# Kernel optimization log

Measured on AMD Instinct MI355X. Metric: run time of the kernel, lower is better.

Reference implementation:

```python
import jax, jax.numpy as jnp
import numpy as np

N, K, C0, H = 256, 16, 16, 32  # vertices, regular degree, input feats, hidden


def setup_inputs() -> dict:
    key = jax.random.key(0)
    ks = jax.random.split(key, 4)
    # k-regular circulant graph: neighbors of i are i+/-1..i+/-K//2 (mod N), sorted by vertex id
    offs = np.concatenate([np.arange(1, K // 2 + 1), -np.arange(1, K // 2 + 1)])
    nbrs = np.sort((np.arange(N)[:, None] + offs[None, :]) % N, axis=1).astype(np.int32)
    X = jax.random.normal(ks[0], (N, C0), jnp.float32)
    W1 = jax.random.normal(ks[1], (18 * C0, H), jnp.float32) / np.sqrt(18 * C0)
    b1 = jnp.zeros((H,), jnp.float32)
    W2 = jax.random.normal(ks[2], (18 * H, H), jnp.float32) / np.sqrt(18 * H)
    b2 = jnp.zeros((H,), jnp.float32)
    fc_w = jax.random.normal(ks[3], (H, 1), jnp.float32) / np.sqrt(H)
    fc_b = jnp.zeros((1,), jnp.float32)
    return {"X": X, "nbrs": jnp.asarray(nbrs), "W1": W1, "b1": b1,
            "W2": W2, "b2": b2, "fc_w": fc_w, "fc_b": fc_b}


def contract18(T, A):
    """All 18 contractions of F6[t,a,b,e,f,c] = T[t,a,b,c] * A[e,f],
    exactly matching _collapse6to3 (_c6to2_111 + _c6to2_12 + _c6to2_3),
    without materializing the 6-d tensor.
    T: (n, k, k, k, c) with axes (vertex, t, a, b, channel); A: (k, k).
    Returns (n, k, k, 18*c)."""
    S = A.sum()            # total sum of A
    r = A.sum(1)           # row sums
    tr = jnp.trace(A)
    sum_b = T.sum(3)              # (n,t,a,c)
    sum_t = T.sum(1)              # (n,a,b,c)
    sum_ab = T.sum((2, 3))        # (n,t,c)
    sum_tb = T.sum((1, 3))        # (n,a,c)
    sum_all = T.sum((1, 2, 3))    # (n,c)
    # _c6to2_111 (5 permutations)
    c1 = sum_b * S
    c2 = sum_ab[:, :, None, :] * r[None, None, :, None]
    c3 = sum_t * S
    c4 = sum_tb[:, :, None, :] * r[None, None, :, None]
    c5 = sum_all[:, None, None, :] * A[None, :, :, None]
    # _c6to2_12 (1 nontrivial permutation + 9 identical identity permutations)
    c6 = jnp.einsum('ntabc,b->ntac', T, r)
    c7 = sum_b * tr  # repeated 9 times, as in the source
    # _c6to2_3 (3 planar-diagonal contractions)
    d_ab = jnp.diagonal(T, axis1=2, axis2=3).transpose(0, 1, 3, 2)   # (n,t,a,c): T[t,a,a,c]
    c16 = jnp.einsum('ntac,ea->ntec', d_ab, A)
    d_tb = jnp.diagonal(T, axis1=1, axis2=3)                          # (n,a,c,t): T[t,a,t,c]
    c17 = jnp.einsum('nact,et->naec', d_tb, A)
    d_ttt = jnp.einsum('ntttc->ntc', T).sum(1)                        # (n,c)
    c18 = d_ttt[:, None, None, :] * A[None, :, :, None]
    return jnp.concatenate([c1, c2, c3, c4, c5, c6] + [c7] * 9 + [c16, c17, c18], axis=-1)


def _forward(X, nbrs, W1, b1, W2, b2, fc_w, fc_b):
    n, k = nbrs.shape
    # chi_{i,t}[a,p] = 1 iff a-th neighbor of i == p-th neighbor of j, j = nbrs[i,t]
    NN = nbrs[nbrs]                                                    # (n,k,k)
    CH = (nbrs[:, None, :, None] == NN[:, :, None, :]).astype(X.dtype)  # (n,t,a,p)
    A = jnp.eye(k, dtype=X.dtype)  # chi_{i,i} is the k x k identity for every i

    # get_F0: broadcast vertex features to (n, k, k, c0)
    F = jnp.broadcast_to(X[:, None, None, :], (n, k, k, X.shape[1]))

    def layer(F, W, b):
        Fg = F[nbrs]                                             # (n,t,p,q,c) gather neighbor features
        tmp = jnp.einsum('ntap,ntpqc->ntaqc', CH, Fg)            # chi @ F
        T = jnp.einsum('ntaqc,ntbq->ntabc', tmp, CH)             # (chi @ F) @ chi^T
        col = contract18(T, A)                                   # (n,k,k,18c)
        return jax.nn.relu(col @ W + b)

    F1 = layer(F, W1, b1)
    F2 = layer(F1, W2, b2)
    # get_Troot then full sum: chi_root scatters F2 entries injectively into [n,n,c],
    # so sum over Troot == sum over all entries of F2.
    g = F2.sum((0, 1, 2))                                        # (H,)
    return g @ fc_w + fc_b                                       # (1,)


def reference(X, nbrs, W1, b1, W2, b2, fc_w, fc_b):
    return _forward(X, nbrs, W1, b1, W2, b2, fc_w, fc_b)
```

## Files before the change

### kernel.cpp

```cpp
#include <hip/hip_runtime.h>


constexpr int KN = 16, HH = 32, NV = 256, C2 = 32;

#define MM_SL(WPTR, NB, COEF_EXPR, ACC) do {                                   \
    const float4* W4_ = (const float4*)(WPTR);                                 \
    _Pragma("unroll")                                                          \
    for (int B = 0; B < (NB); ++B) {                                           \
        _Pragma("unroll")                                                      \
        for (int cc = 0; cc < 8; ++cc) {                                       \
            const int ci = B * 8 + cc;                                         \
            const float cf_ = (COEF_EXPR);                                     \
            _Pragma("unroll")                                                  \
            for (int h4 = 0; h4 < 8; ++h4) {                                   \
                const float4 w_ = W4_[ci * 8 + h4];                            \
                (ACC)[4*h4+0] = fmaf(cf_, w_.x, (ACC)[4*h4+0]);                \
                (ACC)[4*h4+1] = fmaf(cf_, w_.y, (ACC)[4*h4+1]);                \
                (ACC)[4*h4+2] = fmaf(cf_, w_.z, (ACC)[4*h4+2]);                \
                (ACC)[4*h4+3] = fmaf(cf_, w_.w, (ACC)[4*h4+3]);                \
            }                                                                  \
        }                                                                      \
    }                                                                          \
} while (0)

__global__ __launch_bounds__(512)
void ccn_l1(const float* __restrict__ X, const int* __restrict__ nbrs,
            const float* __restrict__ W1, const float* __restrict__ bias,
            float* __restrict__ F1c, float* __restrict__ outz,
            const float* __restrict__ W2f, float* __restrict__ Wsb2)
{
    __shared__ float sE1[6 * 512];
    __shared__ float sPP2[8 * 256 * 4];
    __shared__ float sX[16][20];
    __shared__ float sV[16][164];
    __shared__ int   s_nbi[16];
    __shared__ int   s_nbj[16][17];
    __shared__ int   s_P[16][16];
    __shared__ int   s_vm[16];
    __shared__ float s_m[16];

    const int tid  = threadIdx.x;
    const int i    = ((blockIdx.x & 7) << 5) | (blockIdx.x >> 3);

    if (blockIdx.x == 0 && tid == 0) outz[0] = 0.f;

    if (blockIdx.x < 2) {
        const int u = (blockIdx.x << 9) | tid;
        float acc = 0.f;
        #pragma unroll
        for (int g = 6; g < 15; ++g) acc += W2f[g * 1024 + u];
        Wsb2[u] = 16.f * W2f[u] + W2f[5 * 1024 + u] + 16.f * acc;
    }

    if (tid < 16) s_nbi[tid] = nbrs[i * 16 + tid];
    __syncthreads();

    if (tid < 256) {
        const int t = tid >> 4, y = tid & 15;
        const int j = s_nbi[t];
        s_nbj[t][y] = nbrs[j * 16 + y];
        sX[t][y]    = X[j * 16 + y];
    } else {
        const int u = tid - 256;
        float acc = 0.f;
        #pragma unroll
        for (int g = 6; g < 15; ++g) acc += W1[g * 512 + u];
        sE1[u]        = 16.f * W1[u] + W1[5 * 512 + u] + 16.f * acc;
        sE1[512 + u]  = W1[512 + u];
        sE1[1024 + u] = W1[15 * 512 + u];
        sE1[2048 + u] = W1[3 * 512 + u];
        sE1[2560 + u] = W1[4 * 512 + u];
    }
    __syncthreads();

    if (tid < 256) {
        const int t = tid >> 4, y = tid & 15;
        const int tgt = s_nbi[y];
        int p = -1;
        #pragma unroll
        for (int q = 0; q < 16; ++q) if (s_nbj[t][q] == tgt) p = q;
        s_P[t][y] = p;
        unsigned long long bal = __ballot(p >= 0);
        if (y == 0) {
            int vm = (int)((bal >> ((t & 3) * 16)) & 0xFFFFull);
            s_vm[t] = vm;
            s_m[t]  = (float)__popc(vm);
        }
    } else {
        const int u = tid;
        float acc = 0.f;
        #pragma unroll
        for (int g = 6; g < 15; ++g) acc += W1[g * 512 + u];
        sE1[u]        = 16.f * W1[u] + W1[5 * 512 + u] + 16.f * acc;
        sE1[512 + u]  = W1[512 + u];
        sE1[1024 + u] = W1[15 * 512 + u];
        sE1[2048 + u] = W1[3 * 512 + u];
        sE1[2560 + u] = W1[4 * 512 + u];
    }
    __syncthreads();

    if (tid < 256) {
        const int t = tid >> 4, y = tid & 15, x = t;
        float Y0[16];
        #pragma unroll
        for (int c4 = 0; c4 < 4; ++c4) {
            float4 v = *(const float4*)&sX[t][4 * c4];
            Y0[4*c4+0] = v.x; Y0[4*c4+1] = v.y; Y0[4*c4+2] = v.z; Y0[4*c4+3] = v.w;
        }
        float Z4[16], Z5[16];
        #pragma unroll
        for (int c = 0; c < 16; ++c) { Z4[c] = 0.f; Z5[c] = 0.f; }
        #pragma unroll
        for (int tp = 0; tp < 16; ++tp) {
            const int vm = s_vm[tp];
            const float mt = s_m[tp];
            const float fb = ((vm >> x) & 1) ? mt : 0.f;
            const float f5 = mt * mt;
            #pragma unroll
            for (int c4 = 0; c4 < 4; ++c4) {
                float4 v = *(const float4*)&sX[tp][4 * c4];
                Z4[4*c4+0] = fmaf(fb, v.x, Z4[4*c4+0]);
                Z4[4*c4+1] = fmaf(fb, v.y, Z4[4*c4+1]);
                Z4[4*c4+2] = fmaf(fb, v.z, Z4[4*c4+2]);
                Z4[4*c4+3] = fmaf(fb, v.w, Z4[4*c4+3]);
                Z5[4*c4+0] = fmaf(f5, v.x, Z5[4*c4+0]);
                Z5[4*c4+1] = fmaf(f5, v.y, Z5[4*c4+1]);
                Z5[4*c4+2] = fmaf(f5, v.z, Z5[4*c4+2]);
                Z5[4*c4+3] = fmaf(f5, v.w, Z5[4*c4+3]);
            }
        }
        const float m = s_m[t];
        float v0a=0.f,v0b=0.f,v1a=0.f,v1b=0.f,v2a=0.f,v2b=0.f;
        float v3a=0.f,v3b=0.f,v4a=0.f,v4b=0.f;
        const float2* Wsb = (const float2*)(sE1 + 0 * 512);
        const float2* Wab = (const float2*)(sE1 + 1 * 512);
        const float2* W16 = (const float2*)(sE1 + 2 * 512);
        const float2* Wtb = (const float2*)(sE1 + 4 * 512);
        const float2* Wal = (const float2*)(sE1 + 5 * 512);
        #pragma unroll
        for (int c = 0; c < 16; ++c) {
            const float cf0 = m * Y0[c];
            const float cf1 = m * cf0;
            const float cf2 = Y0[c];
            const float cf3 = Z4[c];
            const float cf4 = Z5[c];
            const int idx = c * 16 + y;
            float2 w0 = Wsb[idx]; v0a = fmaf(cf0, w0.x, v0a); v0b = fmaf(cf0, w0.y, v0b);
            float2 w1 = Wab[idx]; v1a = fmaf(cf1, w1.x, v1a); v1b = fmaf(cf1, w1.y, v1b);
            float2 w2 = W16[idx]; v2a = fmaf(cf2, w2.x, v2a); v2b = fmaf(cf2, w2.y, v2b);
            float2 w3 = Wtb[idx]; v3a = fmaf(cf3, w3.x, v3a); v3b = fmaf(cf3, w3.y, v3b);
            float2 w4 = Wal[idx]; v4a = fmaf(cf4, w4.x, v4a); v4b = fmaf(cf4, w4.y, v4b);
        }
        *(float2*)&sV[t][0 * 32 + 2 * y] = make_float2(v0a, v0b);
        *(float2*)&sV[t][1 * 32 + 2 * y] = make_float2(v1a, v1b);
        *(float2*)&sV[t][2 * 32 + 2 * y] = make_float2(v2a, v2b);
        *(float2*)&sV[t][3 * 32 + 2 * y] = make_float2(v3a, v3b);
        *(float2*)&sV[t][4 * 32 + 2 * y] = make_float2(v4a, v4b);
    } else {
        const int w = tid - 256;
        const int t = w >> 4, y = w & 15, x = t;
        float Z2[16];
        #pragma unroll
        for (int c = 0; c < 16; ++c) Z2[c] = 0.f;
        #pragma unroll
        for (int tp = 0; tp < 16; ++tp) {
            const int vm = s_vm[tp];
            const float f2 = (float)((vm >> x) & (vm >> y) & 1);
            #pragma unroll
            for (int c4 = 0; c4 < 4; ++c4) {
                float4 v = *(const float4*)&sX[tp][4 * c4];
                Z2[4*c4+0] = fmaf(f2, v.x, Z2[4*c4+0]);
                Z2[4*c4+1] = fmaf(f2, v.y, Z2[4*c4+1]);
                Z2[4*c4+2] = fmaf(f2, v.z, Z2[4*c4+2]);
                Z2[4*c4+3] = fmaf(f2, v.w, Z2[4*c4+3]);
            }
        }
        float pp[HH];
        #pragma unroll
        for (int h = 0; h < HH; ++h) pp[h] = 0.f;
        MM_SL(W1 + 2 * 512, 2, 16.f * Z2[ci], pp);
        const int cell = y * 16 + t;
        #pragma unroll
        for (int h4 = 0; h4 < 8; ++h4)
            *(float4*)&sPP2[(h4 * 256 + cell) * 4] =
                make_float4(pp[4*h4], pp[4*h4+1], pp[4*h4+2], pp[4*h4+3]);
    }
    __syncthreads();

    if (tid < 256) {
        const int q = tid >> 4, p = tid & 15;
        const float vy  = (s_P[p][q] >= 0) ? 1.f : 0.f;
        const float dxy = (p == q) ? 1.f : 0.f;
        float4* F4 = (float4*)F1c;
        const size_t basec = ((size_t)i * 16 + q) * 128 + p;
        #pragma unroll
        for (int h4 = 0; h4 < 8; ++h4) {
            const float4 V0 = *(const float4*)&sV[p][0 * 32 + 4 * h4];
            const float4 V1 = *(const float4*)&sV[p][1 * 32 + 4 * h4];
            const float4 V2 = *(const float4*)&sV[p][2 * 32 + 4 * h4];
            const float4 V3 = *(const float4*)&sV[p][3 * 32 + 4 * h4];
            const float4 V4 = *(const float4*)&sV[p][4 * 32 + 4 * h4];
            const float4 PP = *(const float4*)&sPP2[(h4 * 256 + q * 16 + p) * 4];
            float a_ = vy*(V0.x+V2.x) + V1.x + V3.x + dxy*V4.x + PP.x + bias[4*h4+0];
            float b_ = vy*(V0.y+V2.y) + V1.y + V3.y + dxy*V4.y + PP.y + bias[4*h4+1];
            float c_ = vy*(V0.z+V2.z) + V1.z + V3.z + dxy*V4.z + PP.z + bias[4*h4+2];
            float d_ = vy*(V0.w+V2.w) + V1.w + V3.w + dxy*V4.w + PP.w + bias[4*h4+3];
            F4[basec + h4 * 16] = make_float4(a_ > 0.f ? a_ : 0.f, b_ > 0.f ? b_ : 0.f,
                                              c_ > 0.f ? c_ : 0.f, d_ > 0.f ? d_ : 0.f);
        }
    }
}

__global__ __launch_bounds__(512)
void ccn_l2(const float* __restrict__ F1c, const int* __restrict__ nbrs,
            const float* __restrict__ W2, const float* __restrict__ bias,
            const float* __restrict__ fcw, const float* __restrict__ fcb,
            float* __restrict__ out, const float* __restrict__ Wsb2)
{
    __shared__ float sW3[3 * 1024];
    __shared__ float sRpp[256 * 36];
    __shared__ float s_stb[16 * 33];
    __shared__ float s_sall[C2];
    __shared__ int   s_nbi[16];
    __shared__ int   s_PQ[16 * 17];
    __shared__ float s_red[4];

    const int tid  = threadIdx.x;
    const int i    = ((blockIdx.x & 7) << 5) | (blockIdx.x >> 3);
    const int lane = tid & 63;
    const float4* F4 = (const float4*)F1c;

    if (tid < 16) s_nbi[tid] = nbrs[i * 16 + tid];
    __syncthreads();

    if (tid < 256) {
        const int t = tid >> 4, y = tid & 15;
        const int j = s_nbi[t];
        s_PQ[t * 17 + y] = nbrs[j * 16 + y];
    } else {
        const int w = tid - 256;
        #pragma unroll
        for (int s = 0; s < 4; ++s) {
            const int u = w + s * 256;
            sW3[u]        = W2[1 * 1024 + u];
            sW3[1024 + u] = W2[3 * 1024 + u];
            sW3[2048 + u] = W2[4 * 1024 + u];
        }
    }
    __syncthreads();

    if (tid < 256) {
        const int t = tid >> 4, y = tid & 15;
        const int tgt = s_nbi[y];
        int p = -1;
        #pragma unroll
        for (int q = 0; q < 16; ++q) if (s_PQ[t * 17 + q] == tgt) p = q;
        s_PQ[t * 17 + y] = p;
    }
    __syncthreads();

    float pre[HH];
    float sab[C2];
    float pp[HH];

    if (tid < 256) {
        const int t = tid >> 4, y = tid & 15;
        const int j = s_nbi[t];
        const int p = s_PQ[t * 17 + y];
        const float mp = (p >= 0) ? 1.f : 0.f;
        const int pc = p >= 0 ? p : 0;
        const size_t jbase = (size_t)j * 2048;

        float R[C2];
        #pragma unroll
        for (int c = 0; c < C2; ++c) R[c] = 0.f;
        #pragma unroll
        for (int b = 0; b < 16; ++b) {
            const int q = s_PQ[t * 17 + b];
            const float mm = (q >= 0) ? mp : 0.f;
            const int qc = q >= 0 ? q : 0;
            const size_t rb = jbase + (size_t)qc * 128 + pc;
            #pragma unroll
            for (int c4 = 0; c4 < 8; ++c4) {
                float4 v = F4[rb + c4 * 16];
                R[4*c4+0] = fmaf(mm, v.x, R[4*c4+0]);
                R[4*c4+1] = fmaf(mm, v.y, R[4*c4+1]);
                R[4*c4+2] = fmaf(mm, v.z, R[4*c4+2]);
                R[4*c4+3] = fmaf(mm, v.w, R[4*c4+3]);
            }
        }
        #pragma unroll
        for (int c4 = 0; c4 < 8; ++c4)
            *(float4*)&sRpp[(t * 16 + y) * 36 + 4 * c4] =
                make_float4(R[4*c4+0], R[4*c4+1], R[4*c4+2], R[4*c4+3]);

        #pragma unroll
        for (int h = 0; h < HH; ++h) pre[h] = 0.f;
        MM_SL(Wsb2, 4, R[ci], pre);

        #pragma unroll
        for (int c = 0; c < C2; ++c) {
            float s = R[c];
            s += __shfl_xor(s, 1);
            s += __shfl_xor(s, 2);
            s += __shfl_xor(s, 4);
            s += __shfl_xor(s, 8);
            sab[c] = s;
        }

        float D[C2];
        {
            const size_t db = jbase + (size_t)pc * 128 + pc;
            #pragma unroll
            for (int c4 = 0; c4 < 8; ++c4) {
                float4 v = F4[db + c4 * 16];
                D[4*c4+0] = mp * v.x; D[4*c4+1] = mp * v.y;
                D[4*c4+2] = mp * v.z; D[4*c4+3] = mp * v.w;
            }
        }
        MM_SL(W2 + 15 * 1024, 4, D[ci], pre);
    } else {
        const int w = tid - 256;
        const int g = w >> 4, l = w & 15;
        float ST[C2];
        #pragma unroll
        for (int c = 0; c < C2; ++c) ST[c] = 0.f;
        #pragma unroll
        for (int tp = 0; tp < 16; ++tp) {
            const int jt = s_nbi[tp];
            const int py = s_PQ[tp * 17 + g];
            const int px = s_PQ[tp * 17 + l];
            const float mm = (px >= 0 && py >= 0) ? 1.f : 0.f;
            const int pyc = py >= 0 ? py : 0;
            const int pxc = px >= 0 ? px : 0;
            const size_t rb = (size_t)jt * 2048 + (size_t)pyc * 128 + pxc;
            #pragma unroll
            for (int c4 = 0; c4 < 8; ++c4) {
                float4 v = F4[rb + c4 * 16];
                ST[4*c4+0] = fmaf(mm, v.x, ST[4*c4+0]);
                ST[4*c4+1] = fmaf(mm, v.y, ST[4*c4+1]);
                ST[4*c4+2] = fmaf(mm, v.z, ST[4*c4+2]);
                ST[4*c4+3] = fmaf(mm, v.w, ST[4*c4+3]);
            }
        }
        #pragma unroll
        for (int h = 0; h < HH; ++h) pp[h] = 0.f;
        MM_SL(W2 + 2 * 1024, 4, 16.f * ST[ci], pp);
    }
    __syncthreads();

    if (tid < 256) {
        #pragma unroll
        for (int k = 0; k < 2; ++k) {
            const int x2 = (tid >> 5) + 8 * k;
            const int c = tid & 31;
            float s = 0.f;
            #pragma unroll
            for (int tt = 0; tt < 16; ++tt) s += sRpp[(tt * 16 + x2) * 36 + c];
            s_stb[x2 * 33 + c] = s;
        }
    }
    __syncthreads();

    if (tid < 256) {
        if (tid < 32) {
            float s = 0.f;
            #pragma unroll
            for (int x2 = 0; x2 < 16; ++x2) s += s_stb[x2 * 33 + tid];
            s_sall[tid] = s;
        }
    } else {
        const int w = tid - 256;
        const int g = w >> 4, l = w & 15;
        float* dst = &sRpp[(l * 16 + g) * 36];
        #pragma unroll
        for (int h4 = 0; h4 < 8; ++h4)
            *(float4*)&dst[4 * h4] = make_float4(pp[4*h4], pp[4*h4+1], pp[4*h4+2], pp[4*h4+3]);
    }
    __syncthreads();

    if (tid < 256) {
        const int t = tid >> 4, y = tid & 15, x = t;
        const float dxy = (x == y) ? 1.f : 0.f;
        float S0 = 0.f, S1 = 0.f, L0 = 0.f, L1 = 0.f;
        {
            const float2* Wab = (const float2*)(sW3 + 0 * 1024);
            const float2* Wtb = (const float2*)(sW3 + 1 * 1024);
            const float2* Wal = (const float2*)(sW3 + 2 * 1024);
            #pragma unroll
            for (int c = 0; c < C2; ++c) {
                const float cfa = sab[c];
                const float cft = s_stb[t * 33 + c];
                const float cfl = s_sall[c];
                const int idx = c * 16 + y;
                float2 wa = Wab[idx]; S0 = fmaf(cfa, wa.x, S0); S1 = fmaf(cfa, wa.y, S1);
                float2 wt = Wtb[idx]; S0 = fmaf(cft, wt.x, S0); S1 = fmaf(cft, wt.y, S1);
                float2 wl = Wal[idx]; L0 = fmaf(cfl, wl.x, L0); L1 = fmaf(cfl, wl.y, L1);
            }
        }
        const int gbase = (t & 3) * 16;
        #pragma unroll
        for (int h = 0; h < HH; ++h) {
            const int src = gbase + (h >> 1);
            const float sv = (h & 1) ? S1 : S0;
            const float lv = (h & 1) ? L1 : L0;
            pre[h] += __shfl(sv, src, 64) + dxy * __shfl(lv, src, 64);
        }
        {
            const float* ppr = &sRpp[(t * 16 + y) * 36];
            #pragma unroll
            for (int h4 = 0; h4 < 8; ++h4) {
                const float4 v = *(const float4*)&ppr[4 * h4];
                pre[4*h4+0] += v.x; pre[4*h4+1] += v.y;
                pre[4*h4+2] += v.z; pre[4*h4+3] += v.w;
            }
        }
        float local = 0.f;
        #pragma unroll
        for (int h = 0; h < HH; ++h) {
            float v = pre[h] + bias[h];
            v = v > 0.f ? v : 0.f;
            local += v * fcw[h];
        }
        #pragma unroll
        for (int off = 32; off > 0; off >>= 1) local += __shfl_down(local, off, 64);
        if (lane == 0) s_red[tid >> 6] = local;
    }
    __syncthreads();
    if (tid == 0) {
        const float v = s_red[0] + s_red[1] + s_red[2] + s_red[3]
                      + fcb[0] * (1.f / 256.f);
        atomicAdd(out, v);
    }
}

extern "C" void kernel_launch(void* const* d_in, const int* in_sizes, int n_in,
                              void* d_out, int out_size, void* d_ws, size_t ws_size,
                              hipStream_t stream) {
    const float* X    = (const float*)d_in[0];
    const int*   nbrs = (const int*)  d_in[1];
    const float* W1   = (const float*)d_in[2];
    const float* b1   = (const float*)d_in[3];
    const float* W2   = (const float*)d_in[4];
    const float* b2   = (const float*)d_in[5];
    const float* fc_w = (const float*)d_in[6];
    const float* fc_b = (const float*)d_in[7];
    float* outp = (float*)d_out;

    float* F1c  = (float*)d_ws;
    float* Wsb2 = F1c + 2097152;

    ccn_l1<<<NV, 512, 0, stream>>>(X, nbrs, W1, b1, F1c, outp, W2, Wsb2);
    ccn_l2<<<NV, 512, 0, stream>>>(F1c, nbrs, W2, b2, fc_w, fc_b, outp, Wsb2);
}
```

Measured before the change: 113.6 us.

## Use packed FP32 FMA and stage weight matrices in shared memory

The scalar fmaf accumulation loops in both kernels become v_pk_fma/add/mul_f32 inline assembly on float2 vectors, which halves the VALU instruction count for the dense accumulations. The weight slices consumed by the MM_SL matmuls (W1 block 2, Wsb2, W2 blocks 15 and 2) are now copied into LDS up front and read from there instead of from global memory. This trades more shared memory per block, which may lower occupancy, for less global traffic and fewer arithmetic instructions. Inline asm can also limit how the compiler schedules and allocates registers.

```diff
diff --git a/kernel.cpp b/kernel.cpp
--- a/kernel.cpp
+++ b/kernel.cpp
@@ -3,22 +3,38 @@
 
 constexpr int KN = 16, HH = 32, NV = 256, C2 = 32;
 
-#define MM_SL(WPTR, NB, COEF_EXPR, ACC) do {                                   \
-    const float4* W4_ = (const float4*)(WPTR);                                 \
+typedef float f32x2 __attribute__((ext_vector_type(2)));
+typedef float f32x4 __attribute__((ext_vector_type(4)));
+
+__device__ __forceinline__ f32x2 pkfma(f32x2 a, f32x2 b, f32x2 c) {
+    f32x2 d;
+    asm("v_pk_fma_f32 %0, %1, %2, %3" : "=v"(d) : "v"(a), "v"(b), "v"(c));
+    return d;
+}
+__device__ __forceinline__ f32x2 pkadd(f32x2 a, f32x2 b) {
+    f32x2 d;
+    asm("v_pk_add_f32 %0, %1, %2" : "=v"(d) : "v"(a), "v"(b));
+    return d;
+}
+__device__ __forceinline__ f32x2 pkmul(f32x2 a, f32x2 b) {
+    f32x2 d;
+    asm("v_pk_mul_f32 %0, %1, %2" : "=v"(d) : "v"(a), "v"(b));
+    return d;
+}
+__device__ __forceinline__ f32x2 vlo(f32x4 v) { return __builtin_shufflevector(v, v, 0, 1); }
+__device__ __forceinline__ f32x2 vhi(f32x4 v) { return __builtin_shufflevector(v, v, 2, 3); }
+
+#define MM_DS(WLDS, NC, COEF_EXPR, ACC2) do {                                  \
+    const f32x4* W4_ = (const f32x4*)(WLDS);                                   \
     _Pragma("unroll")                                                          \
-    for (int B = 0; B < (NB); ++B) {                                           \
+    for (int ci = 0; ci < (NC); ++ci) {                                        \
+        const float cfs_ = (COEF_EXPR);                                        \
+        const f32x2 cf2_ = {cfs_, cfs_};                                       \
         _Pragma("unroll")                                                      \
-        for (int cc = 0; cc < 8; ++cc) {                                       \
-            const int ci = B * 8 + cc;                                         \
-            const float cf_ = (COEF_EXPR);                                     \
-            _Pragma("unroll")                                                  \
-            for (int h4 = 0; h4 < 8; ++h4) {                                   \
-                const float4 w_ = W4_[ci * 8 + h4];                            \
-                (ACC)[4*h4+0] = fmaf(cf_, w_.x, (ACC)[4*h4+0]);                \
-                (ACC)[4*h4+1] = fmaf(cf_, w_.y, (ACC)[4*h4+1]);                \
-                (ACC)[4*h4+2] = fmaf(cf_, w_.z, (ACC)[4*h4+2]);                \
-                (ACC)[4*h4+3] = fmaf(cf_, w_.w, (ACC)[4*h4+3]);                \
-            }                                                                  \
+        for (int h4 = 0; h4 < 8; ++h4) {                                       \
+            const f32x4 w_ = W4_[ci * 8 + h4];                                 \
+            (ACC2)[2*h4+0] = pkfma(cf2_, vlo(w_), (ACC2)[2*h4+0]);             \
+            (ACC2)[2*h4+1] = pkfma(cf2_, vhi(w_), (ACC2)[2*h4+1]);             \
         }                                                                      \
     }                                                                          \
 } while (0)
@@ -68,6 +84,7 @@
         sE1[u]        = 16.f * W1[u] + W1[5 * 512 + u] + 16.f * acc;
         sE1[512 + u]  = W1[512 + u];
         sE1[1024 + u] = W1[15 * 512 + u];
+        sE1[1536 + u] = W1[2 * 512 + u];
         sE1[2048 + u] = W1[3 * 512 + u];
         sE1[2560 + u] = W1[4 * 512 + u];
     }
@@ -94,6 +111,7 @@
         sE1[u]        = 16.f * W1[u] + W1[5 * 512 + u] + 16.f * acc;
         sE1[512 + u]  = W1[512 + u];
         sE1[1024 + u] = W1[15 * 512 + u];
+        sE1[1536 + u] = W1[2 * 512 + u];
         sE1[2048 + u] = W1[3 * 512 + u];
         sE1[2560 + u] = W1[4 * 512 + u];
     }
@@ -107,26 +125,24 @@
             float4 v = *(const float4*)&sX[t][4 * c4];
             Y0[4*c4+0] = v.x; Y0[4*c4+1] = v.y; Y0[4*c4+2] = v.z; Y0[4*c4+3] = v.w;
         }
-        float Z4[16], Z5[16];
-        #pragma unroll
-        for (int c = 0; c < 16; ++c) { Z4[c] = 0.f; Z5[c] = 0.f; }
+        f32x2 Z42[8], Z52[8];
+        #pragma unroll
+        for (int c = 0; c < 8; ++c) { Z42[c] = (f32x2){0.f,0.f}; Z52[c] = (f32x2){0.f,0.f}; }
         #pragma unroll
         for (int tp = 0; tp < 16; ++tp) {
             const int vm = s_vm[tp];
             const float mt = s_m[tp];
             const float fb = ((vm >> x) & 1) ? mt : 0.f;
             const float f5 = mt * mt;
+            const f32x2 fb2 = {fb, fb};
+            const f32x2 f52 = {f5, f5};
             #pragma unroll
             for (int c4 = 0; c4 < 4; ++c4) {
-                float4 v = *(const float4*)&sX[tp][4 * c4];
-                Z4[4*c4+0] = fmaf(fb, v.x, Z4[4*c4+0]);
-                Z4[4*c4+1] = fmaf(fb, v.y, Z4[4*c4+1]);
-                Z4[4*c4+2] = fmaf(fb, v.z, Z4[4*c4+2]);
-                Z4[4*c4+3] = fmaf(fb, v.w, Z4[4*c4+3]);
-                Z5[4*c4+0] = fmaf(f5, v.x, Z5[4*c4+0]);
-                Z5[4*c4+1] = fmaf(f5, v.y, Z5[4*c4+1]);
-                Z5[4*c4+2] = fmaf(f5, v.z, Z5[4*c4+2]);
-                Z5[4*c4+3] = fmaf(f5, v.w, Z5[4*c4+3]);
+                const f32x4 v = *(const f32x4*)&sX[tp][4 * c4];
+                Z42[2*c4+0] = pkfma(fb2, vlo(v), Z42[2*c4+0]);
+                Z42[2*c4+1] = pkfma(fb2, vhi(v), Z42[2*c4+1]);
+                Z52[2*c4+0] = pkfma(f52, vlo(v), Z52[2*c4+0]);
+                Z52[2*c4+1] = pkfma(f52, vhi(v), Z52[2*c4+1]);
             }
         }
         const float m = s_m[t];
@@ -142,8 +158,8 @@
             const float cf0 = m * Y0[c];
             const float cf1 = m * cf0;
             const float cf2 = Y0[c];
-            const float cf3 = Z4[c];
-            const float cf4 = Z5[c];
+            const float cf3 = Z42[c >> 1][c & 1];
+            const float cf4 = Z52[c >> 1][c & 1];
             const int idx = c * 16 + y;
             float2 w0 = Wsb[idx]; v0a = fmaf(cf0, w0.x, v0a); v0b = fmaf(cf0, w0.y, v0b);
             float2 w1 = Wab[idx]; v1a = fmaf(cf1, w1.x, v1a); v1b = fmaf(cf1, w1.y, v1b);
@@ -159,31 +175,32 @@
     } else {
         const int w = tid - 256;
         const int t = w >> 4, y = w & 15, x = t;
-        float Z2[16];
-        #pragma unroll
-        for (int c = 0; c < 16; ++c) Z2[c] = 0.f;
+        f32x2 Z22[8];
+        #pragma unroll
+        for (int c = 0; c < 8; ++c) Z22[c] = (f32x2){0.f,0.f};
         #pragma unroll
         for (int tp = 0; tp < 16; ++tp) {
             const int vm = s_vm[tp];
             const float f2 = (float)((vm >> x) & (vm >> y) & 1);
+            const f32x2 f22 = {f2, f2};
             #pragma unroll
             for (int c4 = 0; c4 < 4; ++c4) {
-                float4 v = *(const float4*)&sX[tp][4 * c4];
-                Z2[4*c4+0] = fmaf(f2, v.x, Z2[4*c4+0]);
-                Z2[4*c4+1] = fmaf(f2, v.y, Z2[4*c4+1]);
-                Z2[4*c4+2] = fmaf(f2, v.z, Z2[4*c4+2]);
-                Z2[4*c4+3] = fmaf(f2, v.w, Z2[4*c4+3]);
-            }
-        }
-        float pp[HH];
-        #pragma unroll
-        for (int h = 0; h < HH; ++h) pp[h] = 0.f;
-        MM_SL(W1 + 2 * 512, 2, 16.f * Z2[ci], pp);
+                const f32x4 v = *(const f32x4*)&sX[tp][4 * c4];
+                Z22[2*c4+0] = pkfma(f22, vlo(v), Z22[2*c4+0]);
+                Z22[2*c4+1] = pkfma(f22, vhi(v), Z22[2*c4+1]);
+            }
+        }
+        f32x2 pp2[16];
+        #pragma unroll
+        for (int h = 0; h < 16; ++h) pp2[h] = (f32x2){0.f,0.f};
+        MM_DS(sE1 + 3 * 512, 16, 16.f * Z22[ci >> 1][ci & 1], pp2);
         const int cell = y * 16 + t;
         #pragma unroll
-        for (int h4 = 0; h4 < 8; ++h4)
-            *(float4*)&sPP2[(h4 * 256 + cell) * 4] =
-                make_float4(pp[4*h4], pp[4*h4+1], pp[4*h4+2], pp[4*h4+3]);
+        for (int h4 = 0; h4 < 8; ++h4) {
+            const int base = (h4 * 256 + cell) * 4;
+            *(f32x2*)&sPP2[base]     = pp2[2*h4+0];
+            *(f32x2*)&sPP2[base + 2] = pp2[2*h4+1];
+        }
     }
     __syncthreads();
 
@@ -191,22 +208,33 @@
         const int q = tid >> 4, p = tid & 15;
         const float vy  = (s_P[p][q] >= 0) ? 1.f : 0.f;
         const float dxy = (p == q) ? 1.f : 0.f;
+        const f32x2 vy2 = {vy, vy}, dxy2 = {dxy, dxy};
         float4* F4 = (float4*)F1c;
         const size_t basec = ((size_t)i * 16 + q) * 128 + p;
         #pragma unroll
         for (int h4 = 0; h4 < 8; ++h4) {
-            const float4 V0 = *(const float4*)&sV[p][0 * 32 + 4 * h4];
-            const float4 V1 = *(const float4*)&sV[p][1 * 32 + 4 * h4];
-            const float4 V2 = *(const float4*)&sV[p][2 * 32 + 4 * h4];
-            const float4 V3 = *(const float4*)&sV[p][3 * 32 + 4 * h4];
-            const float4 V4 = *(const float4*)&sV[p][4 * 32 + 4 * h4];
-            const float4 PP = *(const float4*)&sPP2[(h4 * 256 + q * 16 + p) * 4];
-            float a_ = vy*(V0.x+V2.x) + V1.x + V3.x + dxy*V4.x + PP.x + bias[4*h4+0];
-            float b_ = vy*(V0.y+V2.y) + V1.y + V3.y + dxy*V4.y + PP.y + bias[4*h4+1];
-            float c_ = vy*(V0.z+V2.z) + V1.z + V3.z + dxy*V4.z + PP.z + bias[4*h4+2];
-            float d_ = vy*(V0.w+V2.w) + V1.w + V3.w + dxy*V4.w + PP.w + bias[4*h4+3];
-            F4[basec + h4 * 16] = make_float4(a_ > 0.f ? a_ : 0.f, b_ > 0.f ? b_ : 0.f,
-                                              c_ > 0.f ? c_ : 0.f, d_ > 0.f ? d_ : 0.f);
+            const f32x4 V0 = *(const f32x4*)&sV[p][0 * 32 + 4 * h4];
+            const f32x4 V1 = *(const f32x4*)&sV[p][1 * 32 + 4 * h4];
+            const f32x4 V2 = *(const f32x4*)&sV[p][2 * 32 + 4 * h4];
+            const f32x4 V3 = *(const f32x4*)&sV[p][3 * 32 + 4 * h4];
+            const f32x4 V4 = *(const f32x4*)&sV[p][4 * 32 + 4 * h4];
+            const f32x4 PP = *(const f32x4*)&sPP2[(h4 * 256 + q * 16 + p) * 4];
+            const f32x2 blo = *(const f32x2*)&bias[4 * h4];
+            const f32x2 bhi = *(const f32x2*)&bias[4 * h4 + 2];
+            f32x2 slo = pkadd(vlo(V0), vlo(V2));
+            slo = pkfma(vy2, slo, vlo(V1));
+            slo = pkadd(slo, vlo(V3));
+            slo = pkfma(dxy2, vlo(V4), slo);
+            slo = pkadd(slo, vlo(PP));
+            slo = pkadd(slo, blo);
+            f32x2 shi = pkadd(vhi(V0), vhi(V2));
+            shi = pkfma(vy2, shi, vhi(V1));
+            shi = pkadd(shi, vhi(V3));
+            shi = pkfma(dxy2, vhi(V4), shi);
+            shi = pkadd(shi, vhi(PP));
+            shi = pkadd(shi, bhi);
+            F4[basec + h4 * 16] = make_float4(fmaxf(slo.x, 0.f), fmaxf(slo.y, 0.f),
+                                              fmaxf(shi.x, 0.f), fmaxf(shi.y, 0.f));
         }
     }
 }
@@ -217,6 +245,7 @@
             const float* __restrict__ fcw, const float* __restrict__ fcb,
             float* __restrict__ out, const float* __restrict__ Wsb2)
 {
+    __shared__ float sMM[3 * 1024];
     __shared__ float sW3[3 * 1024];
     __shared__ float sRpp[256 * 36];
     __shared__ float s_stb[16 * 33];
@@ -228,7 +257,7 @@
     const int tid  = threadIdx.x;
     const int i    = ((blockIdx.x & 7) << 5) | (blockIdx.x >> 3);
     const int lane = tid & 63;
-    const float4* F4 = (const float4*)F1c;
+    const f32x4* F4 = (const f32x4*)F1c;
 
     if (tid < 16) s_nbi[tid] = nbrs[i * 16 + tid];
     __syncthreads();
@@ -239,13 +268,12 @@
         s_PQ[t * 17 + y] = nbrs[j * 16 + y];
     } else {
         const int w = tid - 256;
-        #pragma unroll
-        for (int s = 0; s < 4; ++s) {
-            const int u = w + s * 256;
-            sW3[u]        = W2[1 * 1024 + u];
-            sW3[1024 + u] = W2[3 * 1024 + u];
-            sW3[2048 + u] = W2[4 * 1024 + u];
-        }
+        ((f32x4*)sMM)[w]       = ((const f32x4*)Wsb2)[w];
+        ((f32x4*)sMM)[256 + w] = ((const f32x4*)(W2 + 15 * 1024))[w];
+        ((f32x4*)sMM)[512 + w] = ((const f32x4*)(W2 +  2 * 1024))[w];
+        ((f32x4*)sW3)[w]       = ((const f32x4*)(W2 +  1 * 1024))[w];
+        ((f32x4*)sW3)[256 + w] = ((const f32x4*)(W2 +  3 * 1024))[w];
+        ((f32x4*)sW3)[512 + w] = ((const f32x4*)(W2 +  4 * 1024))[w];
     }
     __syncthreads();
 
@@ -259,9 +287,9 @@
     }
     __syncthreads();
 
-    float pre[HH];
+    f32x2 pre2[16];
     float sab[C2];
-    float pp[HH];
+    f32x2 pp2[16];
 
     if (tid < 256) {
         const int t = tid >> 4, y = tid & 15;
@@ -271,36 +299,39 @@
         const int pc = p >= 0 ? p : 0;
         const size_t jbase = (size_t)j * 2048;
 
-        float R[C2];
-        #pragma unroll
-        for (int c = 0; c < C2; ++c) R[c] = 0.f;
+        f32x2 R2[16];
+        #pragma unroll
+        for (int c = 0; c < 16; ++c) R2[c] = (f32x2){0.f, 0.f};
         #pragma unroll
         for (int b = 0; b < 16; ++b) {
             const int q = s_PQ[t * 17 + b];
             const float mm = (q >= 0) ? mp : 0.f;
+            const f32x2 mm2 = {mm, mm};
             const int qc = q >= 0 ? q : 0;
             const size_t rb = jbase + (size_t)qc * 128 + pc;
             #pragma unroll
             for (int c4 = 0; c4 < 8; ++c4) {
-                float4 v = F4[rb + c4 * 16];
-                R[4*c4+0] = fmaf(mm, v.x, R[4*c4+0]);
-                R[4*c4+1] = fmaf(mm, v.y, R[4*c4+1]);
-                R[4*c4+2] = fmaf(mm, v.z, R[4*c4+2]);
-                R[4*c4+3] = fmaf(mm, v.w, R[4*c4+3]);
-            }
-        }
-        #pragma unroll
-        for (int c4 = 0; c4 < 8; ++c4)
-            *(float4*)&sRpp[(t * 16 + y) * 36 + 4 * c4] =
-                make_float4(R[4*c4+0], R[4*c4+1], R[4*c4+2], R[4*c4+3]);
-
-        #pragma unroll
-        for (int h = 0; h < HH; ++h) pre[h] = 0.f;
-        MM_SL(Wsb2, 4, R[ci], pre);
+                const f32x4 v = F4[rb + c4 * 16];
+                R2[2*c4+0] = pkfma(mm2, vlo(v), R2[2*c4+0]);
+                R2[2*c4+1] = pkfma(mm2, vhi(v), R2[2*c4+1]);
+            }
+        }
+        {
+            float* dst = &sRpp[(t * 16 + y) * 36];
+            #pragma unroll
+            for (int c4 = 0; c4 < 8; ++c4) {
+                *(f32x2*)&dst[4*c4]     = R2[2*c4+0];
+                *(f32x2*)&dst[4*c4 + 2] = R2[2*c4+1];
+            }
+        }
+
+        #pragma unroll
+        for (int h = 0; h < 16; ++h) pre2[h] = (f32x2){0.f, 0.f};
+        MM_DS(sMM, 32, R2[ci >> 1][ci & 1], pre2);
 
         #pragma unroll
         for (int c = 0; c < C2; ++c) {
-            float s = R[c];
+            float s = R2[c >> 1][c & 1];
             s += __shfl_xor(s, 1);
             s += __shfl_xor(s, 2);
             s += __shfl_xor(s, 4);
@@ -308,44 +339,44 @@
             sab[c] = s;
         }
 
-        float D[C2];
+        f32x2 D2[16];
         {
+            const f32x2 mp2 = {mp, mp};
             const size_t db = jbase + (size_t)pc * 128 + pc;
             #pragma unroll
             for (int c4 = 0; c4 < 8; ++c4) {
-                float4 v = F4[db + c4 * 16];
-                D[4*c4+0] = mp * v.x; D[4*c4+1] = mp * v.y;
-                D[4*c4+2] = mp * v.z; D[4*c4+3] = mp * v.w;
-            }
-        }
-        MM_SL(W2 + 15 * 1024, 4, D[ci], pre);
+                const f32x4 v = F4[db + c4 * 16];
+                D2[2*c4+0] = pkmul(mp2, vlo(v));
+                D2[2*c4+1] = pkmul(mp2, vhi(v));
+            }
+        }
+        MM_DS(sMM + 1024, 32, D2[ci >> 1][ci & 1], pre2);
     } else {
         const int w = tid - 256;
         const int g = w >> 4, l = w & 15;
-        float ST[C2];
-        #pragma unroll
-        for (int c = 0; c < C2; ++c) ST[c] = 0.f;
+        f32x2 ST2[16];
+        #pragma unroll
+        for (int c = 0; c < 16; ++c) ST2[c] = (f32x2){0.f, 0.f};
         #pragma unroll
         for (int tp = 0; tp < 16; ++tp) {
             const int jt = s_nbi[tp];
             const int py = s_PQ[tp * 17 + g];
             const int px = s_PQ[tp * 17 + l];
             const float mm = (px >= 0 && py >= 0) ? 1.f : 0.f;
+            const f32x2 mm2 = {mm, mm};
             const int pyc = py >= 0 ? py : 0;
             const int pxc = px >= 0 ? px : 0;
             const size_t rb = (size_t)jt * 2048 + (size_t)pyc * 128 + pxc;
             #pragma unroll
             for (int c4 = 0; c4 < 8; ++c4) {
-                float4 v = F4[rb + c4 * 16];
-                ST[4*c4+0] = fmaf(mm, v.x, ST[4*c4+0]);
-                ST[4*c4+1] = fmaf(mm, v.y, ST[4*c4+1]);
-                ST[4*c4+2] = fmaf(mm, v.z, ST[4*c4+2]);
-                ST[4*c4+3] = fmaf(mm, v.w, ST[4*c4+3]);
-            }
-        }
-        #pragma unroll
-        for (int h = 0; h < HH; ++h) pp[h] = 0.f;
-        MM_SL(W2 + 2 * 1024, 4, 16.f * ST[ci], pp);
+                const f32x4 v = F4[rb + c4 * 16];
+                ST2[2*c4+0] = pkfma(mm2, vlo(v), ST2[2*c4+0]);
+                ST2[2*c4+1] = pkfma(mm2, vhi(v), ST2[2*c4+1]);
+            }
+        }
+        #pragma unroll
+        for (int h = 0; h < 16; ++h) pp2[h] = (f32x2){0.f, 0.f};
+        MM_DS(sMM + 2048, 32, 16.f * ST2[ci >> 1][ci & 1], pp2);
     }
     __syncthreads();
 
@@ -374,8 +405,10 @@
         const int g = w >> 4, l = w & 15;
         float* dst = &sRpp[(l * 16 + g) * 36];
         #pragma unroll
-        for (int h4 = 0; h4 < 8; ++h4)
-            *(float4*)&dst[4 * h4] = make_float4(pp[4*h4], pp[4*h4+1], pp[4*h4+2], pp[4*h4+3]);
+        for (int h4 = 0; h4 < 8; ++h4) {
+            *(f32x2*)&dst[4*h4]     = pp2[2*h4+0];
+            *(f32x2*)&dst[4*h4 + 2] = pp2[2*h4+1];
+        }
     }
     __syncthreads();
 
@@ -404,21 +437,22 @@
             const int src = gbase + (h >> 1);
             const float sv = (h & 1) ? S1 : S0;
             const float lv = (h & 1) ? L1 : L0;
-            pre[h] += __shfl(sv, src, 64) + dxy * __shfl(lv, src, 64);
+            pre2[h >> 1][h & 1] += __shfl(sv, src, 64) + dxy * __shfl(lv, src, 64);
         }
         {
             const float* ppr = &sRpp[(t * 16 + y) * 36];
             #pragma unroll
             for (int h4 = 0; h4 < 8; ++h4) {
-                const float4 v = *(const float4*)&ppr[4 * h4];
-                pre[4*h4+0] += v.x; pre[4*h4+1] += v.y;
-                pre[4*h4+2] += v.z; pre[4*h4+3] += v.w;
+                const f32x2 a = *(const f32x2*)&ppr[4*h4];
+                const f32x2 b = *(const f32x2*)&ppr[4*h4 + 2];
+                pre2[2*h4+0] = pkadd(pre2[2*h4+0], a);
+                pre2[2*h4+1] = pkadd(pre2[2*h4+1], b);
             }
         }
         float local = 0.f;
         #pragma unroll
         for (int h = 0; h < HH; ++h) {
-            float v = pre[h] + bias[h];
+            float v = pre2[h >> 1][h & 1] + bias[h];
             v = v > 0.f ? v : 0.f;
             local += v * fcw[h];
         }
```

After: 104.6 us. 7.9% less time.
